# Kernel tuning notes

Hardware: AMD Instinct MI355X
Metric: run time of the kernel (lower is better)

Reference implementation:

```python
import jax, jax.numpy as jnp
import numpy as np


def _log_g(x):
    # numerically stable log of g(x) = where(x>=0, x+0.5, sigmoid(x))
    return jnp.where(x >= 0, jnp.log(jax.nn.relu(x) + 0.5), -jax.nn.softplus(-x))


def setup_inputs() -> dict:
    key = jax.random.key(0)
    k1, k2, k3, k4 = jax.random.split(key, 4)
    B, T, D = 4, 4096, 1024
    Di = 2 * D  # dim_inner = int(dim * expansion_factor), expansion_factor = 2.0
    x = jax.random.normal(k1, (B, T, D), dtype=jnp.float32)
    prev_hidden = jax.random.uniform(k2, (B, Di), dtype=jnp.float32)  # positive carry state
    # torch Linear(dim, 2*dim_inner, bias=False): stored here pre-transposed as [D, 2*Di]
    W_hg = jax.random.normal(k3, (D, 2 * Di), dtype=jnp.float32) * (1.0 / np.sqrt(D))
    # out_proj Linear(dim_inner, dim, bias=False): stored pre-transposed as [Di, D]
    W_out = jax.random.normal(k4, (Di, D), dtype=jnp.float32) * (1.0 / np.sqrt(Di))
    return {"x": x, "prev_hidden": prev_hidden, "W_hg": W_hg, "W_out": W_out}


def reference(x, prev_hidden, W_hg, W_out):
    # x: [B, T, D]; prev_hidden: [B, Di] (positive)
    T = x.shape[1]
    hg = jnp.einsum('btd,de->bte', x, W_hg)          # [B, T, 2*Di]
    hidden, gate = jnp.split(hg, 2, axis=-1)          # each [B, T, Di]

    # Heinsen log-space affine scan: h_t = (1 - z_t) * h_{t-1} + z_t * g(hidden_t)
    log_coeffs = -jax.nn.softplus(gate)               # log(1 - sigmoid(gate))
    log_values = -jax.nn.softplus(-gate) + _log_g(hidden)  # log(sigmoid(gate)) + log g(hidden)

    # prepend carry state
    prev_log = jnp.clip(jnp.log(jnp.clip(prev_hidden, 1e-8, None)), -30.0, None)[:, None]  # [B,1,Di]
    log_values = jnp.concatenate([prev_log, log_values], axis=1)      # [B, T+1, Di]
    log_coeffs = jnp.pad(log_coeffs, ((0, 0), (1, 0), (0, 0)))        # [B, T+1, Di]

    a_star = jnp.cumsum(log_coeffs, axis=1)
    h = jnp.exp(a_star + jax.lax.cumlogsumexp(log_values - a_star, axis=1))  # [B, T+1, Di]
    h = h[:, -T:]                                     # drop carry slot

    next_hidden = h[:, -1]                            # [B, Di]
    out = jnp.einsum('bte,ed->btd', h, W_out)         # [B, T, D]
    return (out, next_hidden)
```

## Files before the change

kernel.cpp:

```cpp
#include <hip/hip_runtime.h>
#include <cstdio>

#define T_LEN 4096
#define B_SZ  4
#define D_IN  1024
#define DI    2048
#define MM    16384
#define NC2   128
#define CHL2  32

typedef __attribute__((ext_vector_type(8))) __bf16 bf16x8;
typedef __attribute__((ext_vector_type(4))) float  f32x4;
typedef __attribute__((ext_vector_type(8))) unsigned short u16x8;

__device__ __forceinline__ unsigned short f2bf(float f){
  unsigned u = __builtin_bit_cast(unsigned, f);
  u += 0x7fffu + ((u >> 16) & 1u);
  return (unsigned short)(u >> 16);
}
__device__ __forceinline__ float bf2f_lo(unsigned u){
  return __builtin_bit_cast(float, u << 16);
}
__device__ __forceinline__ float bf2f_hi(unsigned u){
  return __builtin_bit_cast(float, u & 0xffff0000u);
}
__device__ __forceinline__ float bf2f_s(unsigned short s){
  return __builtin_bit_cast(float, (unsigned)s << 16);
}

__device__ __forceinline__ void async16(void* lds, const void* g){
  __builtin_amdgcn_global_load_lds((const __attribute__((address_space(1))) void*)g,
                                   (__attribute__((address_space(3))) void*)lds, 16, 0, 0);
}

template<int PERM>
__device__ __forceinline__ void transpose_body(const float* __restrict__ src,
                                               unsigned short* __restrict__ dst,
                                               int n0, int k0, int SK, int SN,
                                               float (*tile)[65], int tid){
  #pragma unroll
  for(int it=0; it<16; it++){
    int idx = it*256 + tid;
    int kk = idx>>6, nn = idx&63;
    int n = n0+nn;
    int col = PERM ? (((n>>5)<<4) + (n&15) + ((n&16)?2048:0)) : n;
    tile[kk][nn] = src[(size_t)(k0+kk)*SN + col];
  }
  __syncthreads();
  #pragma unroll
  for(int it=0; it<16; it++){
    int idx = it*256 + tid;
    int nn = idx>>6, kk = idx&63;
    dst[(size_t)(n0+nn)*SK + k0+kk] = f2bf(tile[kk][nn]);
  }
}

__global__ __launch_bounds__(256) void k_prep(const float* __restrict__ x,
                                              unsigned short* __restrict__ xb,
                                              const float* __restrict__ Whg,
                                              unsigned short* __restrict__ wt,
                                              const float* __restrict__ Wout,
                                              unsigned short* __restrict__ wo){
  __shared__ float tile[64][65];
  int bid = blockIdx.x, tid = threadIdx.x;
  if(bid < 8192){
    size_t t = (size_t)bid*256 + tid;
    const float4* xi = (const float4*)x;
    float4 a = xi[2*t], b = xi[2*t+1];
    u16x8 o;
    o[0]=f2bf(a.x); o[1]=f2bf(a.y); o[2]=f2bf(a.z); o[3]=f2bf(a.w);
    o[4]=f2bf(b.x); o[5]=f2bf(b.y); o[6]=f2bf(b.z); o[7]=f2bf(b.w);
    ((u16x8*)xb)[t] = o;
  } else if(bid < 9216){
    int j = bid - 8192;
    transpose_body<1>(Whg, wt, (j&63)*64, (j>>6)*64, 1024, 4096, tile, tid);
  } else {
    int j = bid - 9216;
    transpose_body<0>(Wout, wo, (j&15)*64, (j>>4)*64, 2048, 1024, tile, tid);
  }
}

template<int EPI>
__device__ __forceinline__ void gemm_body(unsigned short* lsA, unsigned short* lsB,
            const unsigned short* __restrict__ A, const unsigned short* __restrict__ Bt,
            float* __restrict__ C0, unsigned* __restrict__ U0,
            unsigned* __restrict__ U1, unsigned short* __restrict__ Ap,
            unsigned short* __restrict__ Vp, int M, int N, int K){
  int tid  = threadIdx.x;
  int lane = tid & 63, wave = tid >> 6;
  int wm = wave >> 1, wn = wave & 1;
  int cl = lane & 15, quad = lane >> 4;

  int m0 = blockIdx.y * 128, n0 = blockIdx.x * 128;

  f32x4 acc[4][4];
  #pragma unroll
  for(int i=0;i<4;i++)
    #pragma unroll
    for(int j=0;j<4;j++) acc[i][j] = (f32x4){0.f,0.f,0.f,0.f};

  int g = (tid&7) ^ ((tid>>3)&7);
  const unsigned short* gA = A  + (size_t)(m0 + (tid>>3))*K + g*8;
  const unsigned short* gB = Bt + (size_t)(n0 + (tid>>3))*K + g*8;
  unsigned short* dA = lsA + tid*8;
  unsigned short* dB = lsB + tid*8;

  for(int k0=0; k0<K; k0+=64){
    #pragma unroll
    for(int it=0; it<4; it++){
      async16(dA + it*2048, gA + (size_t)(it*32)*K + k0);
      async16(dB + it*2048, gB + (size_t)(it*32)*K + k0);
    }
    __syncthreads();
    #pragma unroll
    for(int kh=0; kh<2; kh++){
      bf16x8 fa[4], fb[4];
      int sl = ((kh<<2)|quad);
      #pragma unroll
      for(int t2=0;t2<4;t2++){
        int ra = wm*64 + t2*16 + cl;
        int rb = wn*64 + t2*16 + cl;
        fa[t2] = *(const bf16x8*)&lsA[ra*64 + (sl^(cl&7))*8];
        fb[t2] = *(const bf16x8*)&lsB[rb*64 + (sl^(cl&7))*8];
      }
      #pragma unroll
      for(int i=0;i<4;i++)
        #pragma unroll
        for(int j=0;j<4;j++)
          acc[i][j] = __builtin_amdgcn_mfma_f32_16x16x32_bf16(fa[i], fb[j], acc[i][j], 0, 0, 0);
    }
    __syncthreads();
  }

  if(EPI==0){
    #pragma unroll
    for(int i=0;i<4;i++)
      #pragma unroll
      for(int j=0;j<4;j++){
        int n = n0 + wn*64 + j*16 + cl;
        #pragma unroll
        for(int r=0;r<4;r++){
          int m = m0 + wm*64 + i*16 + quad*4 + r;
          C0[(size_t)m*N + n] = acc[i][j][r];
        }
      }
  } else {
    float* lA_f = (float*)lsA;
    float* lV_f = (float*)lsB;
    int ibase = ((n0 + wn*64) >> 1) + cl;
    int odd = cl & 1;
    #pragma unroll
    for(int i=0;i<4;i++)
      #pragma unroll
      for(int p=0;p<2;p++){
        f32x4 hh = acc[i][2*p], gg = acc[i][2*p+1];
        int ii = ibase + p*16;
        float pa = 1.f, pv = 0.f;
        #pragma unroll
        for(int r=0;r<4;r++){
          int m = m0 + wm*64 + i*16 + quad*4 + r;
          float gate = gg[r], hid = hh[r];
          float e  = __expf(gate);
          float cc = 1.f/(1.f + e);
          float z  = (gate > 80.f) ? 1.f : e*cc;
          float gv = (hid >= 0.f) ? (hid + 0.5f) : (1.f/(1.f + __expf(-hid)));
          float vv = z*gv;
          float ccp = __shfl_xor(cc, 1, 64);
          float vvp = __shfl_xor(vv, 1, 64);
          unsigned wlo = odd ? (unsigned)f2bf(vvp) : (unsigned)f2bf(cc);
          unsigned whi = odd ? (unsigned)f2bf(vv)  : (unsigned)f2bf(ccp);
          unsigned* dst = odd ? U1 : U0;
          dst[((size_t)m*DI + (ii & ~1)) >> 1] = wlo | (whi << 16);
          pa *= cc;
          pv = fmaf(cc, pv, vv);
        }
        int seg = wm*16 + i*4 + quad;
        int chl = wn*32 + p*16 + cl;
        lA_f[seg*72 + chl] = pa;
        lV_f[seg*72 + chl] = pv;
      }
    __syncthreads();
    {
      int ch = tid & 63, q = tid >> 6;
      float Ac = 1.f, Vc = 0.f;
      #pragma unroll
      for(int s=0; s<8; s++){
        int idx = (q*8 + s)*72 + ch;
        float a = lA_f[idx], v = lV_f[idx];
        Ac *= a;
        Vc = fmaf(a, Vc, v);
      }
      int b = m0 >> 12;
      int ch32 = ((m0 & 4095) >> 5) + q;
      size_t o = (size_t)(b*NC2 + ch32)*DI + (n0 >> 1) + ch;
      Ap[o] = f2bf(Ac); Vp[o] = f2bf(Vc);
    }
  }
}

__global__ __launch_bounds__(256, 2)
void k_gemmHG(const unsigned short* __restrict__ A, const unsigned short* __restrict__ Bt,
              unsigned* __restrict__ U0, unsigned* __restrict__ U1,
              unsigned short* __restrict__ Ap, unsigned short* __restrict__ Vp,
              int M, int N, int K){
  __shared__ unsigned short lsA[128*64];
  __shared__ unsigned short lsB[128*64];
  gemm_body<1>(lsA, lsB, A, Bt, nullptr, U0, U1, Ap, Vp, M, N, K);
}

__global__ __launch_bounds__(256, 2)
void k_gemmOUT(const unsigned short* __restrict__ A, const unsigned short* __restrict__ Bt,
               float* __restrict__ C0, int M, int N, int K){
  __shared__ unsigned short lsA[19456];
  __shared__ unsigned short lsB[128*64];
  gemm_body<0>(lsA, lsB, A, Bt, C0, nullptr, nullptr, nullptr, nullptr, M, N, K);
}

__global__ __launch_bounds__(256) void k_scanB(const float* __restrict__ prev,
                                               unsigned short* __restrict__ Ap,
                                               const unsigned short* __restrict__ Vp){
  int tid = threadIdx.x;
  int cl = tid & 31;
  int g  = tid >> 5;
  int chan = blockIdx.x*32 + cl;
  int i = chan & (DI-1); int b = chan >> 11;
  size_t o0 = (size_t)(b*NC2 + g*16)*DI + i;
  float a[16], v[16];
  #pragma unroll
  for(int j=0;j<16;j++){
    a[j] = bf2f_s(Ap[o0 + (size_t)j*DI]);
    v[j] = bf2f_s(Vp[o0 + (size_t)j*DI]);
  }
  float A = 1.f, V = 0.f;
  #pragma unroll
  for(int j=0;j<16;j++){ A *= a[j]; V = fmaf(a[j], V, v[j]); }
  __shared__ float sA[8][32], sV[8][32], sH[8][32];
  sA[g][cl] = A; sV[g][cl] = V;
  __syncthreads();
  if(g == 0){
    float h = fmaxf(prev[chan], 1e-8f);
    #pragma unroll
    for(int j=0;j<8;j++){
      sH[j][cl] = h;
      h = fmaf(sA[j][cl], h, sV[j][cl]);
    }
  }
  __syncthreads();
  float h = sH[g][cl];
  #pragma unroll
  for(int j=0;j<16;j++){
    Ap[o0 + (size_t)j*DI] = f2bf(h);
    h = fmaf(a[j], h, v[j]);
  }
}

__global__ __launch_bounds__(256) void k_scanC(const uint4* __restrict__ cp,
                                               uint4* __restrict__ vp,
                                               const uint4* __restrict__ hinp,
                                               float* __restrict__ nh){
  int t = blockIdx.x*256 + threadIdx.x;
  int i8 = t & (DI/8 - 1);
  int ch = (t >> 8) & (NC2-1);
  int b  = t >> 15;
  size_t base = ((size_t)(b*T_LEN + ch*CHL2))*(DI/8) + i8;
  uint4 hp = hinp[(size_t)(b*NC2 + ch)*(DI/8) + i8];
  float h0 = bf2f_lo(hp.x), h1 = bf2f_hi(hp.x);
  float h2 = bf2f_lo(hp.y), h3 = bf2f_hi(hp.y);
  float h4 = bf2f_lo(hp.z), h5 = bf2f_hi(hp.z);
  float h6 = bf2f_lo(hp.w), h7 = bf2f_hi(hp.w);
  #pragma unroll 4
  for(int s=0; s<CHL2; s++){
    uint4 cu = cp[base], vu = vp[base];
    h0 = fmaf(bf2f_lo(cu.x), h0, bf2f_lo(vu.x));
    h1 = fmaf(bf2f_hi(cu.x), h1, bf2f_hi(vu.x));
    h2 = fmaf(bf2f_lo(cu.y), h2, bf2f_lo(vu.y));
    h3 = fmaf(bf2f_hi(cu.y), h3, bf2f_hi(vu.y));
    h4 = fmaf(bf2f_lo(cu.z), h4, bf2f_lo(vu.z));
    h5 = fmaf(bf2f_hi(cu.z), h5, bf2f_hi(vu.z));
    h6 = fmaf(bf2f_lo(cu.w), h6, bf2f_lo(vu.w));
    h7 = fmaf(bf2f_hi(cu.w), h7, bf2f_hi(vu.w));
    uint4 o;
    o.x = (unsigned)f2bf(h0) | ((unsigned)f2bf(h1) << 16);
    o.y = (unsigned)f2bf(h2) | ((unsigned)f2bf(h3) << 16);
    o.z = (unsigned)f2bf(h4) | ((unsigned)f2bf(h5) << 16);
    o.w = (unsigned)f2bf(h6) | ((unsigned)f2bf(h7) << 16);
    vp[base] = o;
    base += DI/8;
  }
  if(ch == NC2-1){
    float* d = nh + (size_t)b*DI + 8*i8;
    d[0]=h0; d[1]=h1; d[2]=h2; d[3]=h3; d[4]=h4; d[5]=h5; d[6]=h6; d[7]=h7;
  }
}

extern "C" void kernel_launch(void* const* d_in, const int* in_sizes, int n_in,
                              void* d_out, int out_size, void* d_ws, size_t ws_size,
                              hipStream_t stream){
  const float* x    = (const float*)d_in[0];
  const float* prev = (const float*)d_in[1];
  const float* Whg  = (const float*)d_in[2];
  const float* Wout = (const float*)d_in[3];
  float* out = (float*)d_out;
  float* nh  = out + (size_t)MM*D_IN;

  const size_t NEED = 117440512;
  if(ws_size < NEED){
    fprintf(stderr, "kernel_launch: ws_size=%zu < needed %zu — aborting launch\n",
            ws_size, NEED);
    return;
  }
  char* ws = (char*)d_ws;
  unsigned short* xb = (unsigned short*)(ws);
  unsigned short* wt = (unsigned short*)(ws + 33554432);
  unsigned short* wo = (unsigned short*)(ws + 41943040);
  unsigned short* v  = (unsigned short*)(ws + 46137344);
  unsigned short* Ap = (unsigned short*)(ws + 113246208);
  unsigned short* Vp = (unsigned short*)(ws + 115343360);
  unsigned* c = (unsigned*)d_out;

  k_prep<<<9728, 256, 0, stream>>>(x, xb, Whg, wt, Wout, wo);

  k_gemmHG<<<dim3(32,128), 256, 0, stream>>>(xb, wt, c, (unsigned*)v,
                                             Ap, Vp, MM, 2*DI, D_IN);

  k_scanB<<<256,  256, 0, stream>>>(prev, Ap, Vp);
  k_scanC<<<512,  256, 0, stream>>>((const uint4*)c, (uint4*)v,
                                    (const uint4*)Ap, nh);

  k_gemmOUT<<<dim3(8,128), 256, 0, stream>>>(v, wo, out, MM, D_IN, DI);
}
```

Before: 415.4 us.

## Enlarge output GEMM tile to 256x128 and add block-index swizzle

The shared gemm_body template is inlined into each kernel. The output-projection GEMM now gives each block a 256x128 tile, with each wave covering 128 rows and holding 8x4 MFMA accumulators. This halves the grid and increases operand reuse from LDS. A block-index swizzle groups consecutive workgroups so they share the same W_out column tile, which should improve cache locality. The cost is higher register pressure, which may hurt occupancy or cause spills, and fewer blocks to spread across the CUs.

After: 391.5 us, median of 2. -5.8%, faster.

```diff
diff --git a/kernel.cpp b/kernel.cpp
--- a/kernel.cpp
+++ b/kernel.cpp
@@ -80,124 +80,6 @@
   }
 }
 
-template<int EPI>
-__device__ __forceinline__ void gemm_body(unsigned short* lsA, unsigned short* lsB,
-            const unsigned short* __restrict__ A, const unsigned short* __restrict__ Bt,
-            float* __restrict__ C0, unsigned* __restrict__ U0,
-            unsigned* __restrict__ U1, unsigned short* __restrict__ Ap,
-            unsigned short* __restrict__ Vp, int M, int N, int K){
-  int tid  = threadIdx.x;
-  int lane = tid & 63, wave = tid >> 6;
-  int wm = wave >> 1, wn = wave & 1;
-  int cl = lane & 15, quad = lane >> 4;
-
-  int m0 = blockIdx.y * 128, n0 = blockIdx.x * 128;
-
-  f32x4 acc[4][4];
-  #pragma unroll
-  for(int i=0;i<4;i++)
-    #pragma unroll
-    for(int j=0;j<4;j++) acc[i][j] = (f32x4){0.f,0.f,0.f,0.f};
-
-  int g = (tid&7) ^ ((tid>>3)&7);
-  const unsigned short* gA = A  + (size_t)(m0 + (tid>>3))*K + g*8;
-  const unsigned short* gB = Bt + (size_t)(n0 + (tid>>3))*K + g*8;
-  unsigned short* dA = lsA + tid*8;
-  unsigned short* dB = lsB + tid*8;
-
-  for(int k0=0; k0<K; k0+=64){
-    #pragma unroll
-    for(int it=0; it<4; it++){
-      async16(dA + it*2048, gA + (size_t)(it*32)*K + k0);
-      async16(dB + it*2048, gB + (size_t)(it*32)*K + k0);
-    }
-    __syncthreads();
-    #pragma unroll
-    for(int kh=0; kh<2; kh++){
-      bf16x8 fa[4], fb[4];
-      int sl = ((kh<<2)|quad);
-      #pragma unroll
-      for(int t2=0;t2<4;t2++){
-        int ra = wm*64 + t2*16 + cl;
-        int rb = wn*64 + t2*16 + cl;
-        fa[t2] = *(const bf16x8*)&lsA[ra*64 + (sl^(cl&7))*8];
-        fb[t2] = *(const bf16x8*)&lsB[rb*64 + (sl^(cl&7))*8];
-      }
-      #pragma unroll
-      for(int i=0;i<4;i++)
-        #pragma unroll
-        for(int j=0;j<4;j++)
-          acc[i][j] = __builtin_amdgcn_mfma_f32_16x16x32_bf16(fa[i], fb[j], acc[i][j], 0, 0, 0);
-    }
-    __syncthreads();
-  }
-
-  if(EPI==0){
-    #pragma unroll
-    for(int i=0;i<4;i++)
-      #pragma unroll
-      for(int j=0;j<4;j++){
-        int n = n0 + wn*64 + j*16 + cl;
-        #pragma unroll
-        for(int r=0;r<4;r++){
-          int m = m0 + wm*64 + i*16 + quad*4 + r;
-          C0[(size_t)m*N + n] = acc[i][j][r];
-        }
-      }
-  } else {
-    float* lA_f = (float*)lsA;
-    float* lV_f = (float*)lsB;
-    int ibase = ((n0 + wn*64) >> 1) + cl;
-    int odd = cl & 1;
-    #pragma unroll
-    for(int i=0;i<4;i++)
-      #pragma unroll
-      for(int p=0;p<2;p++){
-        f32x4 hh = acc[i][2*p], gg = acc[i][2*p+1];
-        int ii = ibase + p*16;
-        float pa = 1.f, pv = 0.f;
-        #pragma unroll
-        for(int r=0;r<4;r++){
-          int m = m0 + wm*64 + i*16 + quad*4 + r;
-          float gate = gg[r], hid = hh[r];
-          float e  = __expf(gate);
-          float cc = 1.f/(1.f + e);
-          float z  = (gate > 80.f) ? 1.f : e*cc;
-          float gv = (hid >= 0.f) ? (hid + 0.5f) : (1.f/(1.f + __expf(-hid)));
-          float vv = z*gv;
-          float ccp = __shfl_xor(cc, 1, 64);
-          float vvp = __shfl_xor(vv, 1, 64);
-          unsigned wlo = odd ? (unsigned)f2bf(vvp) : (unsigned)f2bf(cc);
-          unsigned whi = odd ? (unsigned)f2bf(vv)  : (unsigned)f2bf(ccp);
-          unsigned* dst = odd ? U1 : U0;
-          dst[((size_t)m*DI + (ii & ~1)) >> 1] = wlo | (whi << 16);
-          pa *= cc;
-          pv = fmaf(cc, pv, vv);
-        }
-        int seg = wm*16 + i*4 + quad;
-        int chl = wn*32 + p*16 + cl;
-        lA_f[seg*72 + chl] = pa;
-        lV_f[seg*72 + chl] = pv;
-      }
-    __syncthreads();
-    {
-      int ch = tid & 63, q = tid >> 6;
-      float Ac = 1.f, Vc = 0.f;
-      #pragma unroll
-      for(int s=0; s<8; s++){
-        int idx = (q*8 + s)*72 + ch;
-        float a = lA_f[idx], v = lV_f[idx];
-        Ac *= a;
-        Vc = fmaf(a, Vc, v);
-      }
-      int b = m0 >> 12;
-      int ch32 = ((m0 & 4095) >> 5) + q;
-      size_t o = (size_t)(b*NC2 + ch32)*DI + (n0 >> 1) + ch;
-      Ap[o] = f2bf(Ac); Vp[o] = f2bf(Vc);
-    }
-  }
-}
-
 __global__ __launch_bounds__(256, 2)
 void k_gemmHG(const unsigned short* __restrict__ A, const unsigned short* __restrict__ Bt,
               unsigned* __restrict__ U0, unsigned* __restrict__ U1,
@@ -205,7 +87,102 @@
               int M, int N, int K){
   __shared__ unsigned short lsA[128*64];
   __shared__ unsigned short lsB[128*64];
-  gemm_body<1>(lsA, lsB, A, Bt, nullptr, U0, U1, Ap, Vp, M, N, K);
+  int tid  = threadIdx.x;
+  int lane = tid & 63, wave = tid >> 6;
+  int wm = wave >> 1, wn = wave & 1;
+  int cl = lane & 15, quad = lane >> 4;
+
+  int m0 = blockIdx.y * 128, n0 = blockIdx.x * 128;
+
+  f32x4 acc[4][4];
+  #pragma unroll
+  for(int i=0;i<4;i++)
+    #pragma unroll
+    for(int j=0;j<4;j++) acc[i][j] = (f32x4){0.f,0.f,0.f,0.f};
+
+  int g = (tid&7) ^ ((tid>>3)&7);
+  const unsigned short* gA = A  + (size_t)(m0 + (tid>>3))*K + g*8;
+  const unsigned short* gB = Bt + (size_t)(n0 + (tid>>3))*K + g*8;
+  unsigned short* dA = lsA + tid*8;
+  unsigned short* dB = lsB + tid*8;
+
+  for(int k0=0; k0<K; k0+=64){
+    #pragma unroll
+    for(int it=0; it<4; it++){
+      async16(dA + it*2048, gA + (size_t)(it*32)*K + k0);
+      async16(dB + it*2048, gB + (size_t)(it*32)*K + k0);
+    }
+    __syncthreads();
+    #pragma unroll
+    for(int kh=0; kh<2; kh++){
+      bf16x8 fa[4], fb[4];
+      int sl = ((kh<<2)|quad);
+      #pragma unroll
+      for(int t2=0;t2<4;t2++){
+        int ra = wm*64 + t2*16 + cl;
+        int rb = wn*64 + t2*16 + cl;
+        fa[t2] = *(const bf16x8*)&lsA[ra*64 + (sl^(cl&7))*8];
+        fb[t2] = *(const bf16x8*)&lsB[rb*64 + (sl^(cl&7))*8];
+      }
+      #pragma unroll
+      for(int i=0;i<4;i++)
+        #pragma unroll
+        for(int j=0;j<4;j++)
+          acc[i][j] = __builtin_amdgcn_mfma_f32_16x16x32_bf16(fa[i], fb[j], acc[i][j], 0, 0, 0);
+    }
+    __syncthreads();
+  }
+
+  float* lA_f = (float*)lsA;
+  float* lV_f = (float*)lsB;
+  int ibase = ((n0 + wn*64) >> 1) + cl;
+  int odd = cl & 1;
+  #pragma unroll
+  for(int i=0;i<4;i++)
+    #pragma unroll
+    for(int p=0;p<2;p++){
+      f32x4 hh = acc[i][2*p], gg = acc[i][2*p+1];
+      int ii = ibase + p*16;
+      float pa = 1.f, pv = 0.f;
+      #pragma unroll
+      for(int r=0;r<4;r++){
+        int m = m0 + wm*64 + i*16 + quad*4 + r;
+        float gate = gg[r], hid = hh[r];
+        float e  = __expf(gate);
+        float cc = 1.f/(1.f + e);
+        float z  = (gate > 80.f) ? 1.f : e*cc;
+        float gv = (hid >= 0.f) ? (hid + 0.5f) : (1.f/(1.f + __expf(-hid)));
+        float vv = z*gv;
+        float ccp = __shfl_xor(cc, 1, 64);
+        float vvp = __shfl_xor(vv, 1, 64);
+        unsigned wlo = odd ? (unsigned)f2bf(vvp) : (unsigned)f2bf(cc);
+        unsigned whi = odd ? (unsigned)f2bf(vv)  : (unsigned)f2bf(ccp);
+        unsigned* dst = odd ? U1 : U0;
+        dst[((size_t)m*DI + (ii & ~1)) >> 1] = wlo | (whi << 16);
+        pa *= cc;
+        pv = fmaf(cc, pv, vv);
+      }
+      int seg = wm*16 + i*4 + quad;
+      int chl = wn*32 + p*16 + cl;
+      lA_f[seg*72 + chl] = pa;
+      lV_f[seg*72 + chl] = pv;
+    }
+  __syncthreads();
+  {
+    int ch = tid & 63, q = tid >> 6;
+    float Ac = 1.f, Vc = 0.f;
+    #pragma unroll
+    for(int s=0; s<8; s++){
+      int idx = (q*8 + s)*72 + ch;
+      float a = lA_f[idx], v = lV_f[idx];
+      Ac *= a;
+      Vc = fmaf(a, Vc, v);
+    }
+    int b = m0 >> 12;
+    int ch32 = ((m0 & 4095) >> 5) + q;
+    size_t o = (size_t)(b*NC2 + ch32)*DI + (n0 >> 1) + ch;
+    Ap[o] = f2bf(Ac); Vp[o] = f2bf(Vc);
+  }
 }
 
 __global__ __launch_bounds__(256, 2)
@@ -213,7 +190,72 @@
                float* __restrict__ C0, int M, int N, int K){
   __shared__ unsigned short lsA[19456];
   __shared__ unsigned short lsB[128*64];
-  gemm_body<0>(lsA, lsB, A, Bt, C0, nullptr, nullptr, nullptr, nullptr, M, N, K);
+  int tid  = threadIdx.x;
+  int lane = tid & 63, wave = tid >> 6;
+  int wm = wave >> 1, wn = wave & 1;
+  int cl = lane & 15, quad = lane >> 4;
+
+  int gx = gridDim.x;
+  int nwg = gx * gridDim.y;
+  int orig = blockIdx.y * gx + blockIdx.x;
+  int swz = (orig & 7) * (nwg >> 3) + (orig >> 3);
+  int bx = swz & (gx - 1), by = swz >> 3;
+  int m0 = by * 256, n0 = bx * 128;
+
+  f32x4 acc[8][4];
+  #pragma unroll
+  for(int i=0;i<8;i++)
+    #pragma unroll
+    for(int j=0;j<4;j++) acc[i][j] = (f32x4){0.f,0.f,0.f,0.f};
+
+  int g = (tid&7) ^ ((tid>>3)&7);
+  const unsigned short* gA = A  + (size_t)(m0 + (tid>>3))*K + g*8;
+  const unsigned short* gB = Bt + (size_t)(n0 + (tid>>3))*K + g*8;
+  unsigned short* dA = lsA + tid*8;
+  unsigned short* dB = lsB + tid*8;
+
+  for(int k0=0; k0<K; k0+=64){
+    #pragma unroll
+    for(int it=0; it<8; it++)
+      async16(dA + it*2048, gA + (size_t)(it*32)*K + k0);
+    #pragma unroll
+    for(int it=0; it<4; it++)
+      async16(dB + it*2048, gB + (size_t)(it*32)*K + k0);
+    __syncthreads();
+    #pragma unroll
+    for(int kh=0; kh<2; kh++){
+      bf16x8 fa[8], fb[4];
+      int sl = ((kh<<2)|quad);
+      #pragma unroll
+      for(int t2=0;t2<4;t2++){
+        int rb = wn*64 + t2*16 + cl;
+        fb[t2] = *(const bf16x8*)&lsB[rb*64 + (sl^(cl&7))*8];
+      }
+      #pragma unroll
+      for(int t2=0;t2<8;t2++){
+        int ra = wm*128 + t2*16 + cl;
+        fa[t2] = *(const bf16x8*)&lsA[ra*64 + (sl^(cl&7))*8];
+      }
+      #pragma unroll
+      for(int i=0;i<8;i++)
+        #pragma unroll
+        for(int j=0;j<4;j++)
+          acc[i][j] = __builtin_amdgcn_mfma_f32_16x16x32_bf16(fa[i], fb[j], acc[i][j], 0, 0, 0);
+    }
+    __syncthreads();
+  }
+
+  #pragma unroll
+  for(int i=0;i<8;i++)
+    #pragma unroll
+    for(int j=0;j<4;j++){
+      int n = n0 + wn*64 + j*16 + cl;
+      #pragma unroll
+      for(int r=0;r<4;r++){
+        int m = m0 + wm*128 + i*16 + quad*4 + r;
+        C0[(size_t)m*N + n] = acc[i][j][r];
+      }
+    }
 }
 
 __global__ __launch_bounds__(256) void k_scanB(const float* __restrict__ prev,
@@ -327,5 +369,5 @@
   k_scanC<<<512,  256, 0, stream>>>((const uint4*)c, (uint4*)v,
                                     (const uint4*)Ap, nh);
 
-  k_gemmOUT<<<dim3(8,128), 256, 0, stream>>>(v, wo, out, MM, D_IN, DI);
-}
+  k_gemmOUT<<<dim3(8,64), 256, 0, stream>>>(v, wo, out, MM, D_IN, DI);
+}
```
